# Kernel optimization log

Hardware: AMD Instinct MI355X
Metric: run time of the kernel (lower is better)

Reference implementation:

```python
import jax, jax.numpy as jnp
import numpy as np

B, T, D = 8, 2048, 1024
H, C, DV = 8, 64, 128   # n_heads, latent_dim, d_head
LN_EPS = 1e-5
NORM_EPS = 1e-12  # F.normalize eps


def _xavier(k, shape, fan_in, fan_out):
    lim = float(np.sqrt(6.0 / (fan_in + fan_out)))
    return jax.random.uniform(k, shape, jnp.float32, -lim, lim)


def setup_inputs() -> dict:
    key = jax.random.key(0)
    ks = jax.random.split(key, 9)
    x = jax.random.normal(ks[0], (B, T, D), jnp.float32)
    Wq = _xavier(ks[1], (C, D), D, C)            # S_q weight (out,in)
    Wk = _xavier(ks[2], (C, D), D, C)            # S_k
    Wv = _xavier(ks[3], (C, D), D, C)            # S_v
    Qc = _xavier(ks[4], (H, C, C), C, C)         # per-head latent rotations
    Vc = _xavier(ks[5], (H, C, DV), C, DV)       # per-head value up-proj
    Wa_w = _xavier(ks[6], (H * C, D), D, H * C)  # W_alpha weight
    Wa_b = jnp.full((H * C,), 3.0, jnp.float32)  # W_alpha bias init = 3.0
    Wo = _xavier(ks[7], (D, H * DV), H * DV, D)  # output proj
    gamma = jnp.ones((D,), jnp.float32)
    beta = jnp.zeros((D,), jnp.float32)
    return {"x": x, "Wq": Wq, "Wk": Wk, "Wv": Wv, "Qc": Qc, "Vc": Vc,
            "Wa_w": Wa_w, "Wa_b": Wa_b, "Wo": Wo, "gamma": gamma, "beta": beta}


def _forward(x, Wq, Wk, Wv, Qc, Vc, Wa_w, Wa_b, Wo, gamma, beta):
    residual = x
    # LayerNorm (biased variance, like torch)
    mu = jnp.mean(x, axis=-1, keepdims=True)
    var = jnp.mean(jnp.square(x - mu), axis=-1, keepdims=True)
    xn = (x - mu) * jax.lax.rsqrt(var + LN_EPS) * gamma + beta

    q_lat = xn @ Wq.T          # (B,T,C)
    k_lat = xn @ Wk.T          # (B,T,C) shared across heads
    v_lat = xn @ Wv.T          # (B,T,C)

    q = jnp.einsum('btc,hce->bhte', q_lat, Qc)   # (B,H,T,C)
    v = jnp.einsum('btc,hcd->bhtd', v_lat, Vc)   # (B,H,T,DV)
    alpha = jax.nn.sigmoid(xn @ Wa_w.T + Wa_b)   # (B,T,H*C)
    alpha = alpha.reshape(x.shape[0], x.shape[1], H, C).transpose(0, 2, 1, 3)  # (B,H,T,C)

    # F.normalize(k, dim=-1): k / max(||k||, eps)
    kn = k_lat / jnp.maximum(jnp.linalg.norm(k_lat, axis=-1, keepdims=True), NORM_EPS)

    # time-major for scan
    qs = jnp.moveaxis(q, 2, 0)      # (T,B,H,C)
    vs = jnp.moveaxis(v, 2, 0)      # (T,B,H,DV)
    als = jnp.moveaxis(alpha, 2, 0)  # (T,B,H,C)
    kns = jnp.moveaxis(kn, 1, 0)    # (T,B,C)

    S0 = jnp.zeros((x.shape[0], H, C, DV), x.dtype)

    def step(S, inp):
        q_t, k_t, v_t, a_t = inp
        # S_t = diag(alpha_t) S_{t-1} + k_t v_t^T  (k shared across heads)
        S = a_t[..., None] * S + k_t[:, None, :, None] * v_t[..., None, :]
        o_t = jnp.einsum('bhcv,bhc->bhv', S, q_t)
        return S, o_t

    _, outs = jax.lax.scan(step, S0, (qs, kns, vs, als))  # outs: (T,B,H,DV)
    out = jnp.moveaxis(outs, 0, 1).reshape(x.shape[0], x.shape[1], H * DV)
    return out @ Wo.T + residual


def reference(x, Wq, Wk, Wv, Qc, Vc, Wa_w, Wa_b, Wo, gamma, beta):
    return _forward(x, Wq, Wk, Wv, Qc, Vc, Wa_w, Wa_b, Wo, gamma, beta)
```

## Files before the change

### kernel.cpp

```cpp
#include <hip/hip_runtime.h>

typedef unsigned short u16;
typedef unsigned int   u32;
typedef __bf16 bf16x8 __attribute__((ext_vector_type(8)));
typedef float  f32x4  __attribute__((ext_vector_type(4)));
typedef float  f32x8  __attribute__((ext_vector_type(8)));

#define B_  8
#define T_  2048
#define D_  1024
#define H_  8
#define C_  64
#define DV_ 128
#define M_  (B_*T_)
#define L_  128
#define NC_ (T_/L_)

__device__ __forceinline__ u16 f2bf(float f){
  u32 u = __float_as_uint(f);
  u32 r = (u + 0x7fffu + ((u >> 16) & 1u)) >> 16;
  return (u16)r;
}
__device__ __forceinline__ float bf2f(u16 u){
  return __uint_as_float(((u32)u) << 16);
}

typedef const __attribute__((address_space(1))) unsigned int* gp1_t;
typedef __attribute__((address_space(3))) unsigned int* lp3_t;
__device__ __forceinline__ void stage16(const void* g, void* l){
  __builtin_amdgcn_global_load_lds((gp1_t)g, (lp3_t)l, 16, 0, 0);
}

__global__ __launch_bounds__(256) void ln_kernel(
    const float* __restrict__ x, const float* __restrict__ gamma,
    const float* __restrict__ beta, u16* __restrict__ xnb){
  const int m = blockIdx.x;
  const int tid = threadIdx.x;
  const int wave = tid >> 6, lane = tid & 63;
  const float* xr = x + (size_t)m * D_;
  float4 xv = *(const float4*)&xr[tid*4];
  float s = xv.x + xv.y + xv.z + xv.w;
  #pragma unroll
  for (int off = 32; off > 0; off >>= 1) s += __shfl_xor(s, off, 64);
  __shared__ float red[8];
  if (lane == 0) red[wave] = s;
  __syncthreads();
  float mu = (red[0]+red[1]+red[2]+red[3]) * (1.f/1024.f);
  float dx = xv.x-mu, dy = xv.y-mu, dz = xv.z-mu, dw = xv.w-mu;
  float ss = dx*dx + dy*dy + dz*dz + dw*dw;
  #pragma unroll
  for (int off = 32; off > 0; off >>= 1) ss += __shfl_xor(ss, off, 64);
  if (lane == 0) red[4+wave] = ss;
  __syncthreads();
  float var = (red[4]+red[5]+red[6]+red[7]) * (1.f/1024.f);
  float rs = rsqrtf(var + 1e-5f);
  float4 g  = *(const float4*)&gamma[tid*4];
  float4 bb = *(const float4*)&beta[tid*4];
  ushort4 o4;
  o4.x = f2bf(dx*rs*g.x + bb.x);
  o4.y = f2bf(dy*rs*g.y + bb.y);
  o4.z = f2bf(dz*rs*g.z + bb.z);
  o4.w = f2bf(dw*rs*g.w + bb.w);
  *(ushort4*)&xnb[(size_t)m*D_ + tid*4] = o4;
}

__global__ __launch_bounds__(256) void prep_weights(
    const float* __restrict__ Wq, const float* __restrict__ Wk,
    const float* __restrict__ Wv, const float* __restrict__ Wa,
    const float* __restrict__ Qc, const float* __restrict__ Vc,
    const float* __restrict__ Wo,
    u16* __restrict__ Wcatb, u16* __restrict__ QcTb,
    u16* __restrict__ VcTb,  u16* __restrict__ Wob){
  int idx = blockIdx.x * 256 + threadIdx.x;
  if (idx < 786432){
    int r = idx >> 10, col = idx & 1023;
    float v = 0.f;
    if (r < 64)       v = Wq[(size_t)r*1024 + col];
    else if (r < 128) v = Wk[(size_t)(r-64)*1024 + col];
    else if (r < 192) v = Wv[(size_t)(r-128)*1024 + col];
    else if (r < 704) v = Wa[(size_t)(r-192)*1024 + col];
    Wcatb[idx] = f2bf(v);
  } else if (idx < 819200){
    int i = idx - 786432;
    int n = i >> 6, c = i & 63; int h = n >> 6, e = n & 63;
    QcTb[i] = f2bf(Qc[((size_t)h*64 + c)*64 + e]);
  } else if (idx < 884736){
    int i = idx - 819200;
    int n = i >> 6, c = i & 63; int h = n >> 7, d = n & 127;
    VcTb[i] = f2bf(Vc[((size_t)h*64 + c)*128 + d]);
  } else {
    int i = idx - 884736;
    Wob[i] = f2bf(Wo[i]);
  }
}

__global__ __launch_bounds__(256) void gemm_bf16(
    const u16* __restrict__ A, const u16* __restrict__ Bw,
    float* __restrict__ C, const float* __restrict__ res,
    u16* __restrict__ Cb, int N, int K){
  __shared__ u16 As[128*32];
  __shared__ u16 Bs[128*32];
  const int tid = threadIdx.x;
  const int wave = tid >> 6;
  const int lane = tid & 63;
  const int q  = lane >> 4;
  const int mr = lane & 15;
  const int wr = wave >> 1, wc = wave & 1;
  const int m0 = blockIdx.x * 128;
  const int n0 = blockIdx.y * 128;

  const int j0 = wave*2;
  const int lr = lane >> 2;
  const int lc = (lane & 3) * 8;
  const u16* pa0 = A  + (size_t)(m0 + (j0  )*16 + lr)*K + lc;
  const u16* pa1 = A  + (size_t)(m0 + (j0+1)*16 + lr)*K + lc;
  const u16* pb0 = Bw + (size_t)(n0 + (j0  )*16 + lr)*K + lc;
  const u16* pb1 = Bw + (size_t)(n0 + (j0+1)*16 + lr)*K + lc;
  u16* la0 = &As[(j0  )*512];
  u16* la1 = &As[(j0+1)*512];
  u16* lb0 = &Bs[(j0  )*512];
  u16* lb1 = &Bs[(j0+1)*512];

  union FragU { uint4 u4; bf16x8 v; };
  f32x4 zero = {0.f, 0.f, 0.f, 0.f};
  f32x4 acc[4][4];
  #pragma unroll
  for (int i = 0; i < 4; i++)
    #pragma unroll
    for (int j = 0; j < 4; j++) acc[i][j] = zero;

  const u16* fA = &As[(size_t)(wr*64 + mr)*32 + q*8];
  const u16* fB = &Bs[(size_t)(wc*64 + mr)*32 + q*8];

  for (int k0 = 0; k0 < K; k0 += 32){
    stage16(pa0, la0);
    stage16(pa1, la1);
    stage16(pb0, lb0);
    stage16(pb1, lb1);
    pa0 += 32; pa1 += 32; pb0 += 32; pb1 += 32;
    __syncthreads();
    bf16x8 afr[4], bfr[4];
    #pragma unroll
    for (int mt = 0; mt < 4; mt++){
      FragU f; f.u4 = *(const uint4*)(fA + mt*512);
      afr[mt] = f.v;
    }
    #pragma unroll
    for (int nt = 0; nt < 4; nt++){
      FragU f; f.u4 = *(const uint4*)(fB + nt*512);
      bfr[nt] = f.v;
    }
    #pragma unroll
    for (int mt = 0; mt < 4; mt++)
      #pragma unroll
      for (int nt = 0; nt < 4; nt++)
        acc[mt][nt] = __builtin_amdgcn_mfma_f32_16x16x32_bf16(
            afr[mt], bfr[nt], acc[mt][nt], 0, 0, 0);
    __syncthreads();
  }

  #pragma unroll
  for (int mt = 0; mt < 4; mt++)
    #pragma unroll
    for (int nt = 0; nt < 4; nt++){
      int col = n0 + wc*64 + nt*16 + mr;
      if (col < N){
        #pragma unroll
        for (int r = 0; r < 4; r++){
          int row = m0 + wr*64 + mt*16 + q*4 + r;
          size_t idx = (size_t)row * N + col;
          float v = acc[mt][nt][r];
          if (res) v += res[idx];
          if (Cb) Cb[idx] = f2bf(v);
          else    C[idx] = v;
        }
      }
    }
}

__global__ __launch_bounds__(256) void split_proj(
    const float* __restrict__ proj, const float* __restrict__ Wab,
    u16* __restrict__ qlatb, float* __restrict__ knf,
    u16* __restrict__ vlatb, float* __restrict__ alphaf){
  const int m = blockIdx.x * 4 + (threadIdx.x >> 6);
  const int lane = threadIdx.x & 63;
  const float* pr = proj + (size_t)m * 704;
  qlatb[(size_t)m*64 + lane] = f2bf(pr[lane]);
  float kv = pr[64 + lane];
  float ss = kv * kv;
  #pragma unroll
  for (int off = 32; off > 0; off >>= 1) ss += __shfl_xor(ss, off, 64);
  float nrm = fmaxf(sqrtf(ss), 1e-12f);
  knf[(size_t)m*64 + lane] = kv / nrm;
  vlatb[(size_t)m*64 + lane] = f2bf(pr[128 + lane]);
  #pragma unroll
  for (int j = 0; j < 8; j++){
    int jj = j*64 + lane;
    float av = pr[192 + jj] + Wab[jj];
    alphaf[(size_t)m*512 + jj] = 1.f / (1.f + expf(-av));
  }
}


__global__ __launch_bounds__(512, 8) void scan_pass1(
    const float* __restrict__ knf, const u16* __restrict__ vb,
    const float* __restrict__ alphaf,
    float* __restrict__ Sbuf, float* __restrict__ btot){
  const int ch = blockIdx.x;
  const int bh = blockIdx.y;
  const int b = bh >> 3, h = bh & 7;
  const int tid = threadIdx.x;
  const int w = __builtin_amdgcn_readfirstlane(tid >> 6);
  const int dg = tid & 63;
  const int t0 = ch * L_;

  const float* kp  = knf    + ((size_t)(b*T_ + t0))*64  + w*8;
  const float* ap  = alphaf + ((size_t)(b*T_ + t0))*512 + h*64 + w*8;
  const float* alp = ap + (dg & 7);
  const u32*   vp  = (const u32*)(vb + ((size_t)(b*T_ + t0))*1024 + h*128) + dg;

  float S[8][2];
  #pragma unroll
  for (int j = 0; j < 8; j++){ S[j][0] = 0.f; S[j][1] = 0.f; }
  float bt = 1.f;

  for (int t = 0; t < L_; t += 2){
    f32x8 a0, a1, k0, k1;
    asm volatile(
      "s_load_dwordx8 %0, %4, 0x0\n\t"
      "s_load_dwordx8 %1, %4, 0x800\n\t"
      "s_load_dwordx8 %2, %5, 0x0\n\t"
      "s_load_dwordx8 %3, %5, 0x100\n\t"
      "s_waitcnt lgkmcnt(0)"
      : "=&s"(a0), "=&s"(a1), "=&s"(k0), "=&s"(k1)
      : "s"(ap), "s"(kp));
    float al0 = alp[0], al1 = alp[512];
    u32 vv0 = vp[0], vv1 = vp[512];
    float v00 = __uint_as_float(vv0 << 16);
    float v01 = __uint_as_float(vv0 & 0xffff0000u);
    float v10 = __uint_as_float(vv1 << 16);
    float v11 = __uint_as_float(vv1 & 0xffff0000u);
    #pragma unroll
    for (int j = 0; j < 8; j++){
      S[j][0] = a0[j]*S[j][0] + k0[j]*v00;
      S[j][1] = a0[j]*S[j][1] + k0[j]*v01;
    }
    bt *= al0;
    #pragma unroll
    for (int j = 0; j < 8; j++){
      S[j][0] = a1[j]*S[j][0] + k1[j]*v10;
      S[j][1] = a1[j]*S[j][1] + k1[j]*v11;
    }
    bt *= al1;
    ap += 1024; kp += 128; alp += 1024; vp += 1024;
  }

  float* Sl = Sbuf + ((size_t)bh*NC_ + ch) * (64*128);
  #pragma unroll
  for (int j = 0; j < 8; j++)
    *(float2*)&Sl[(size_t)(w*8+j)*128 + 2*dg] = make_float2(S[j][0], S[j][1]);
  if (dg < 8) btot[((size_t)bh*NC_ + ch)*64 + w*8 + dg] = bt;
}

__global__ __launch_bounds__(256) void scan_combine(
    float* __restrict__ Sbuf, const float* __restrict__ btot){
  const int bh = blockIdx.y;
  const int e  = blockIdx.x * 256 + threadIdx.x;
  float*       Sb  = Sbuf + (size_t)bh*NC_*8192 + e;
  const float* btb = btot + (size_t)bh*NC_*64 + (e >> 7);
  float S = 0.f;
  #pragma unroll
  for (int j = 0; j < NC_; j++){
    float loc = Sb[(size_t)j*8192];
    Sb[(size_t)j*8192] = S;
    if (j < NC_-1) S = btb[j*64] * S + loc;
  }
}

__global__ __launch_bounds__(512, 8) void scan_pass2(
    const float* __restrict__ qf, const float* __restrict__ knf,
    const u16* __restrict__ vb, const float* __restrict__ alphaf,
    const float* __restrict__ Sbuf, u16* __restrict__ ob){
  const int ch = blockIdx.x;
  const int bh = blockIdx.y;
  const int b = bh >> 3, h = bh & 7;
  const int tid = threadIdx.x;
  const int w = __builtin_amdgcn_readfirstlane(tid >> 6);
  const int dg = tid & 63;
  const int t0 = ch * L_;
  __shared__ __align__(16) float sO[2][8][4][128];

  const float* qp = qf     + ((size_t)(b*T_ + t0))*512 + h*64 + w*8;
  const float* kp = knf    + ((size_t)(b*T_ + t0))*64  + w*8;
  const float* ap = alphaf + ((size_t)(b*T_ + t0))*512 + h*64 + w*8;
  const u32*   vp = (const u32*)(vb + ((size_t)(b*T_ + t0))*1024 + h*128) + dg;
  u16* obase = ob + ((size_t)(b*T_ + t0))*1024 + h*128;

  float S[8][2];
  const float* Si = Sbuf + ((size_t)bh*NC_ + ch) * (64*128);
  #pragma unroll
  for (int j = 0; j < 8; j++){
    float2 s2 = *(const float2*)&Si[(size_t)(w*8+j)*128 + 2*dg];
    S[j][0] = s2.x; S[j][1] = s2.y;
  }

  const int rtt = tid >> 7, rdd = tid & 127;

  for (int sb = 0; sb < L_/4; sb++){
    const int p = sb & 1;
    #pragma unroll
    for (int half = 0; half < 2; half++){
      f32x8 a0, a1, k0, k1, q0, q1;
      asm volatile(
        "s_load_dwordx8 %0, %6, 0x0\n\t"
        "s_load_dwordx8 %1, %6, 0x800\n\t"
        "s_load_dwordx8 %2, %7, 0x0\n\t"
        "s_load_dwordx8 %3, %7, 0x100\n\t"
        "s_load_dwordx8 %4, %8, 0x0\n\t"
        "s_load_dwordx8 %5, %8, 0x800\n\t"
        "s_waitcnt lgkmcnt(0)"
        : "=&s"(a0), "=&s"(a1), "=&s"(k0), "=&s"(k1), "=&s"(q0), "=&s"(q1)
        : "s"(ap), "s"(kp), "s"(qp));
      u32 vv0 = vp[0], vv1 = vp[512];
      float v00 = __uint_as_float(vv0 << 16);
      float v01 = __uint_as_float(vv0 & 0xffff0000u);
      float v10 = __uint_as_float(vv1 << 16);
      float v11 = __uint_as_float(vv1 & 0xffff0000u);
      {
        float oa0, oa1, ob0, ob1;
        S[0][0] = a0[0]*S[0][0] + k0[0]*v00;  oa0 = S[0][0]*q0[0];
        S[0][1] = a0[0]*S[0][1] + k0[0]*v01;  oa1 = S[0][1]*q0[0];
        S[1][0] = a0[1]*S[1][0] + k0[1]*v00;  ob0 = S[1][0]*q0[1];
        S[1][1] = a0[1]*S[1][1] + k0[1]*v01;  ob1 = S[1][1]*q0[1];
        #pragma unroll
        for (int j = 2; j < 8; j += 2){
          S[j][0]   = a0[j]*S[j][0]     + k0[j]*v00;    oa0 += S[j][0]*q0[j];
          S[j][1]   = a0[j]*S[j][1]     + k0[j]*v01;    oa1 += S[j][1]*q0[j];
          S[j+1][0] = a0[j+1]*S[j+1][0] + k0[j+1]*v00;  ob0 += S[j+1][0]*q0[j+1];
          S[j+1][1] = a0[j+1]*S[j+1][1] + k0[j+1]*v01;  ob1 += S[j+1][1]*q0[j+1];
        }
        *(float2*)&sO[p][w][half*2+0][2*dg] = make_float2(oa0+ob0, oa1+ob1);
      }
      {
        float oa0, oa1, ob0, ob1;
        S[0][0] = a1[0]*S[0][0] + k1[0]*v10;  oa0 = S[0][0]*q1[0];
        S[0][1] = a1[0]*S[0][1] + k1[0]*v11;  oa1 = S[0][1]*q1[0];
        S[1][0] = a1[1]*S[1][0] + k1[1]*v10;  ob0 = S[1][0]*q1[1];
        S[1][1] = a1[1]*S[1][1] + k1[1]*v11;  ob1 = S[1][1]*q1[1];
        #pragma unroll
        for (int j = 2; j < 8; j += 2){
          S[j][0]   = a1[j]*S[j][0]     + k1[j]*v10;    oa0 += S[j][0]*q1[j];
          S[j][1]   = a1[j]*S[j][1]     + k1[j]*v11;    oa1 += S[j][1]*q1[j];
          S[j+1][0] = a1[j+1]*S[j+1][0] + k1[j+1]*v10;  ob0 += S[j+1][0]*q1[j+1];
          S[j+1][1] = a1[j+1]*S[j+1][1] + k1[j+1]*v11;  ob1 += S[j+1][1]*q1[j+1];
        }
        *(float2*)&sO[p][w][half*2+1][2*dg] = make_float2(oa0+ob0, oa1+ob1);
      }
      ap += 1024; kp += 128; qp += 1024; vp += 1024;
    }
    __syncthreads();
    float o = sO[p][0][rtt][rdd] + sO[p][1][rtt][rdd]
            + sO[p][2][rtt][rdd] + sO[p][3][rtt][rdd]
            + sO[p][4][rtt][rdd] + sO[p][5][rtt][rdd]
            + sO[p][6][rtt][rdd] + sO[p][7][rtt][rdd];
    obase[(size_t)(sb*4 + rtt)*1024 + rdd] = f2bf(o);
  }
}

extern "C" void kernel_launch(void* const* d_in, const int* in_sizes, int n_in,
                              void* d_out, int out_size, void* d_ws, size_t ws_size,
                              hipStream_t stream){
  const float* x     = (const float*)d_in[0];
  const float* Wq    = (const float*)d_in[1];
  const float* Wk    = (const float*)d_in[2];
  const float* Wv    = (const float*)d_in[3];
  const float* Qc    = (const float*)d_in[4];
  const float* Vc    = (const float*)d_in[5];
  const float* Wa_w  = (const float*)d_in[6];
  const float* Wa_b  = (const float*)d_in[7];
  const float* Wo    = (const float*)d_in[8];
  const float* gamma = (const float*)d_in[9];
  const float* beta  = (const float*)d_in[10];
  float* out = (float*)d_out;

  char* ws = (char*)d_ws;
  size_t off = 0;
  auto alloc = [&](size_t bytes) -> void* {
    void* p = ws + off; off += (bytes + 255) & ~(size_t)255; return p;
  };
  char* R1 = (char*)alloc((size_t)M_ * 1024 * 2);
  u16*   xnb  = (u16*)R1;
  u16*   obuf = (u16*)R1;
  char* R2 = (char*)alloc((size_t)M_ * 704 * 4);
  float* proj = (float*)R2;
  float* qf   = (float*)R2;
  float* Sbuf   = (float*)alloc((size_t)64 * NC_ * 8192 * 4);
  u16*   vfb    = (u16*)alloc((size_t)M_ * 1024 * 2);
  float* alphaf = (float*)alloc((size_t)M_ * 512 * 4);
  float* knf    = (float*)alloc((size_t)M_ * 64 * 4);
  u16*   qlatb  = (u16*)alloc((size_t)M_ * 64 * 2);
  u16*   vlatb  = (u16*)alloc((size_t)M_ * 64 * 2);
  u16*   Wcatb  = (u16*)alloc((size_t)768 * 1024 * 2);
  u16*   QcTb   = (u16*)alloc((size_t)512 * 64 * 2);
  u16*   VcTb   = (u16*)alloc((size_t)1024 * 64 * 2);
  u16*   Wob    = (u16*)alloc((size_t)1024 * 1024 * 2);
  float* btotp  = (float*)alloc((size_t)64 * NC_ * 64 * 4);
  (void)ws_size; (void)in_sizes; (void)n_in; (void)out_size;

  ln_kernel<<<dim3(M_), dim3(256), 0, stream>>>(x, gamma, beta, xnb);
  prep_weights<<<dim3(7552), dim3(256), 0, stream>>>(
      Wq, Wk, Wv, Wa_w, Qc, Vc, Wo, Wcatb, QcTb, VcTb, Wob);
  gemm_bf16<<<dim3(M_/128, 6), dim3(256), 0, stream>>>(
      xnb, Wcatb, proj, nullptr, nullptr, 704, 1024);
  split_proj<<<dim3(M_/4), dim3(256), 0, stream>>>(
      proj, Wa_b, qlatb, knf, vlatb, alphaf);
  gemm_bf16<<<dim3(M_/128, 8), dim3(256), 0, stream>>>(
      vlatb, VcTb, nullptr, nullptr, vfb, 1024, 64);
  gemm_bf16<<<dim3(M_/128, 4), dim3(256), 0, stream>>>(
      qlatb, QcTb, qf, nullptr, nullptr, 512, 64);
  scan_pass1<<<dim3(NC_-1, 64), dim3(512), 0, stream>>>(
      knf, vfb, alphaf, Sbuf, btotp);
  scan_combine<<<dim3(32, 64), dim3(256), 0, stream>>>(Sbuf, btotp);
  scan_pass2<<<dim3(NC_, 64), dim3(512), 0, stream>>>(
      qf, knf, vfb, alphaf, Sbuf, obuf);
  gemm_bf16<<<dim3(M_/128, 8), dim3(256), 0, stream>>>(
      obuf, Wob, out, x, nullptr, 1024, 1024);
}
```

Measured before the change: 520.6 us.

## Double-buffer GEMM LDS tiles, swizzle LDS layout, and remap block order

The bf16 GEMM kernel now keeps two LDS buffers, prefetching the next K-slice while MFMAs run on the current one, and drops one barrier per iteration. LDS columns are XOR-swizzled on both the store and the fragment-load side to cut bank conflicts. Block indices are remapped into strided chunks to change L2 reuse across concurrently running tiles. This doubles LDS use per block, and the swizzle assumes the grid size divides by 8.

After: 513.1 us. Within noise of the previous version (-1.4%).

```diff
diff --git a/kernel.cpp b/kernel.cpp
--- a/kernel.cpp
+++ b/kernel.cpp
@@ -98,28 +98,34 @@
     const u16* __restrict__ A, const u16* __restrict__ Bw,
     float* __restrict__ C, const float* __restrict__ res,
     u16* __restrict__ Cb, int N, int K){
-  __shared__ u16 As[128*32];
-  __shared__ u16 Bs[128*32];
+  __shared__ __align__(16) u16 As[2][128*32];
+  __shared__ __align__(16) u16 Bs[2][128*32];
   const int tid = threadIdx.x;
   const int wave = tid >> 6;
   const int lane = tid & 63;
   const int q  = lane >> 4;
   const int mr = lane & 15;
   const int wr = wave >> 1, wc = wave & 1;
-  const int m0 = blockIdx.x * 128;
-  const int n0 = blockIdx.y * 128;
+
+  const int gx = gridDim.x;
+  const int nlin = blockIdx.y * gx + blockIdx.x;
+  const int chunk = (gx * gridDim.y) >> 3;
+  const int swz = (nlin & 7) * chunk + (nlin >> 3);
+  const int m0 = (swz % gx) * 128;
+  const int n0 = (swz / gx) * 128;
 
   const int j0 = wave*2;
   const int lr = lane >> 2;
-  const int lc = (lane & 3) * 8;
-  const u16* pa0 = A  + (size_t)(m0 + (j0  )*16 + lr)*K + lc;
-  const u16* pa1 = A  + (size_t)(m0 + (j0+1)*16 + lr)*K + lc;
-  const u16* pb0 = Bw + (size_t)(n0 + (j0  )*16 + lr)*K + lc;
-  const u16* pb1 = Bw + (size_t)(n0 + (j0+1)*16 + lr)*K + lc;
-  u16* la0 = &As[(j0  )*512];
-  u16* la1 = &As[(j0+1)*512];
-  u16* lb0 = &Bs[(j0  )*512];
-  u16* lb1 = &Bs[(j0+1)*512];
+  const int slg = ((lane & 3) ^ ((lr >> 1) & 3)) * 8;
+  const u16* pa0 = A  + (size_t)(m0 + (j0  )*16 + lr)*K + slg;
+  const u16* pa1 = A  + (size_t)(m0 + (j0+1)*16 + lr)*K + slg;
+  const u16* pb0 = Bw + (size_t)(n0 + (j0  )*16 + lr)*K + slg;
+  const u16* pb1 = Bw + (size_t)(n0 + (j0+1)*16 + lr)*K + slg;
+  u16* la0 = &As[0][(j0  )*512];
+  u16* la1 = &As[0][(j0+1)*512];
+  u16* lb0 = &Bs[0][(j0  )*512];
+  u16* lb1 = &Bs[0][(j0+1)*512];
+  const int bufstride = 128*32;
 
   union FragU { uint4 u4; bf16x8 v; };
   f32x4 zero = {0.f, 0.f, 0.f, 0.f};
@@ -129,25 +135,32 @@
     #pragma unroll
     for (int j = 0; j < 4; j++) acc[i][j] = zero;
 
-  const u16* fA = &As[(size_t)(wr*64 + mr)*32 + q*8];
-  const u16* fB = &Bs[(size_t)(wc*64 + mr)*32 + q*8];
-
+  const int qs = (q ^ ((mr >> 1) & 3)) * 8;
+  const int aoff = (wr*64 + mr)*32 + qs;
+  const int boff = (wc*64 + mr)*32 + qs;
+
+  stage16(pa0, la0); stage16(pa1, la1);
+  stage16(pb0, lb0); stage16(pb1, lb1);
+  __syncthreads();
+
+  int p = 0;
   for (int k0 = 0; k0 < K; k0 += 32){
-    stage16(pa0, la0);
-    stage16(pa1, la1);
-    stage16(pb0, lb0);
-    stage16(pb1, lb1);
-    pa0 += 32; pa1 += 32; pb0 += 32; pb1 += 32;
-    __syncthreads();
+    if (k0 + 32 < K){
+      int pn = p ^ 1;
+      stage16(pa0 + k0 + 32, la0 + pn*bufstride);
+      stage16(pa1 + k0 + 32, la1 + pn*bufstride);
+      stage16(pb0 + k0 + 32, lb0 + pn*bufstride);
+      stage16(pb1 + k0 + 32, lb1 + pn*bufstride);
+    }
     bf16x8 afr[4], bfr[4];
     #pragma unroll
     for (int mt = 0; mt < 4; mt++){
-      FragU f; f.u4 = *(const uint4*)(fA + mt*512);
+      FragU f; f.u4 = *(const uint4*)(&As[p][aoff + mt*512]);
       afr[mt] = f.v;
     }
     #pragma unroll
     for (int nt = 0; nt < 4; nt++){
-      FragU f; f.u4 = *(const uint4*)(fB + nt*512);
+      FragU f; f.u4 = *(const uint4*)(&Bs[p][boff + nt*512]);
       bfr[nt] = f.v;
     }
     #pragma unroll
@@ -157,6 +170,7 @@
         acc[mt][nt] = __builtin_amdgcn_mfma_f32_16x16x32_bf16(
             afr[mt], bfr[nt], acc[mt][nt], 0, 0, 0);
     __syncthreads();
+    p ^= 1;
   }
 
   #pragma unroll
```
